# Kernel optimization log

Measured on AMD Instinct MI355X. Metric: run time of the kernel, lower is better.

Reference implementation:

```python
import jax, jax.numpy as jnp
import numpy as np

W_, H_, D_ = 45, 30, 13
TEXT = 226
NVID = W_ * H_ * D_            # 17550 video tokens
L = TEXT + NVID                # 17776 total tokens
BLK = 128
NKEEP = 32
NBLK = (L + BLK - 1) // BLK    # 139 blocks
LPAD = NBLK * BLK              # 17792
LEVELS = (1, 2, 4, 8)
MASK_RATIOS = ((1, 0.0, 0.05), (2, 0.05, 0.15), (4, 0.15, 0.25), (8, 0.25, 0.5), (0, 0.5, 1.0))
NEG = -1e30

def _sgn(x):
    return (x > 0) - (x < 0)

def _gen3d(x, y, z, ax, ay, az, bx, by, bz, cx, cy, cz):
    w = abs(ax + ay + az); h = abs(bx + by + bz); d = abs(cx + cy + cz)
    dax, day, daz = _sgn(ax), _sgn(ay), _sgn(az)
    dbx, dby, dbz = _sgn(bx), _sgn(by), _sgn(bz)
    dcx, dcy, dcz = _sgn(cx), _sgn(cy), _sgn(cz)
    if h == 1 and d == 1:
        for _ in range(w):
            yield (x, y, z); x += dax; y += day; z += daz
        return
    if w == 1 and d == 1:
        for _ in range(h):
            yield (x, y, z); x += dbx; y += dby; z += dbz
        return
    if w == 1 and h == 1:
        for _ in range(d):
            yield (x, y, z); x += dcx; y += dcy; z += dcz
        return
    ax2, ay2, az2 = ax // 2, ay // 2, az // 2
    bx2, by2, bz2 = bx // 2, by // 2, bz // 2
    cx2, cy2, cz2 = cx // 2, cy // 2, cz // 2
    w2 = abs(ax2 + ay2 + az2); h2 = abs(bx2 + by2 + bz2); d2 = abs(cx2 + cy2 + cz2)
    if (w2 % 2) and (w > 2): ax2 += dax; ay2 += day; az2 += daz
    if (h2 % 2) and (h > 2): bx2 += dbx; by2 += dby; bz2 += dbz
    if (d2 % 2) and (d > 2): cx2 += dcx; cy2 += dcy; cz2 += dcz
    if (2 * w > 3 * h) and (2 * w > 3 * d):
        yield from _gen3d(x, y, z, ax2, ay2, az2, bx, by, bz, cx, cy, cz)
        yield from _gen3d(x + ax2, y + ay2, z + az2, ax - ax2, ay - ay2, az - az2, bx, by, bz, cx, cy, cz)
    elif 3 * h > 4 * d:
        yield from _gen3d(x, y, z, bx2, by2, bz2, cx, cy, cz, ax2, ay2, az2)
        yield from _gen3d(x + bx2, y + by2, z + bz2, ax, ay, az, bx - bx2, by - by2, bz - bz2, cx, cy, cz)
        yield from _gen3d(x + (ax - dax) + (bx2 - dbx), y + (ay - day) + (by2 - dby), z + (az - daz) + (bz2 - dbz), -bx2, -by2, -bz2, cx, cy, cz, -(ax - ax2), -(ay - ay2), -(az - az2))
    elif 3 * d > 4 * h:
        yield from _gen3d(x, y, z, cx2, cy2, cz2, ax2, ay2, az2, bx, by, bz)
        yield from _gen3d(x + cx2, y + cy2, z + cz2, ax, ay, az, bx, by, bz, cx - cx2, cy - cy2, cz - cz2)
        yield from _gen3d(x + (ax - dax) + (cx2 - dcx), y + (ay - day) + (cy2 - dcy), z + (az - daz) + (cz2 - dcz), -cx2, -cy2, -cz2, -(ax - ax2), -(ay - ay2), -(az - az2), bx, by, bz)
    else:
        yield from _gen3d(x, y, z, bx2, by2, bz2, cx2, cy2, cz2, ax2, ay2, az2)
        yield from _gen3d(x + bx2, y + by2, z + bz2, cx, cy, cz, ax2, ay2, az2, bx - bx2, by - by2, bz - bz2)
        yield from _gen3d(x + (bx2 - dbx) + (cx - dcx), y + (by2 - dby) + (cy - dcy), z + (bz2 - dbz) + (cz - dcz), ax, ay, az, -bx2, -by2, -bz2, -(cx - cx2), -(cy - cy2), -(cz - cz2))
        yield from _gen3d(x + (ax - dax) + bx2 + (cx - dcx), y + (ay - day) + by2 + (cy - dcy), z + (az - daz) + bz2 + (cz - dcz), -cx, -cy, -cz, -(ax - ax2), -(ay - ay2), -(az - az2), bx - bx2, by - by2, bz - bz2)

def _gilbert3d(w, h, d):
    if w >= h and w >= d:
        yield from _gen3d(0, 0, 0, w, 0, 0, 0, h, 0, 0, 0, d)
    elif h >= w and h >= d:
        yield from _gen3d(0, 0, 0, 0, h, 0, w, 0, 0, 0, 0, d)
    else:
        yield from _gen3d(0, 0, 0, 0, 0, d, w, 0, 0, 0, h, 0)

def _perms():
    o2g = np.zeros(NVID, np.int64); g2o = np.zeros(NVID, np.int64)
    for g, (x, y, z) in enumerate(_gilbert3d(W_, H_, D_)):
        c = x + W_ * (y + H_ * z)
        o2g[g] = c; g2o[c] = g
    return jnp.asarray(o2g), jnp.asarray(g2o)

O2G, G2O = _perms()

def _sample(x, key):
    # random_sample_tokens: same NKEEP indices (per b,h) reused for every block
    B, Hh, _, Dd = x.shape
    r = jax.random.uniform(key, (B, Hh, BLK))
    idx = jax.lax.top_k(r, NKEEP)[1]                    # [B,H,NKEEP]
    xb = x.reshape(B, Hh, NBLK, BLK, Dd)
    s = jnp.take_along_axis(xb, idx[:, :, None, :, None], axis=3)
    return s.reshape(B, Hh, NBLK * NKEEP, Dd)

def _make_mask(q, k):
    # torch.no_grad() mask path
    q = jax.lax.stop_gradient(q); k = jax.lax.stop_gradient(k)
    pad = LPAD - L
    qp = jnp.pad(q, ((0, 0), (0, 0), (0, pad), (0, 0)), mode='edge')
    kp = jnp.pad(k, ((0, 0), (0, 0), (0, pad), (0, 0)), mode='edge')
    kq, kk = jax.random.split(jax.random.key(0))
    sq = _sample(qp, kq); sk = _sample(kp, kk)
    scale = 1.0 / float(np.sqrt(q.shape[-1]))
    attn = jax.nn.softmax(jnp.einsum('bhid,bhjd->bhij', sq, sk) * scale, axis=-1)
    B, Hh = attn.shape[:2]
    # sum-pool NKEEP x NKEEP -> block-level pooled attention [B,H,NBLK,NBLK]
    pool = attn.reshape(B, Hh, NBLK, NKEEP, NBLK, NKEEP).sum(axis=(3, 5))
    # rank of each column within its row (descending) == scatter over sorted indices
    rank = jnp.argsort(jnp.argsort(-pool, axis=-1), axis=-1)
    mask = jnp.zeros(pool.shape, jnp.int32)
    for val, s, e in MASK_RATIOS:
        si = max(0, int(NBLK * s)); ei = min(NBLK, int(NBLK * e))
        if si < ei and val != 0:
            mask = jnp.where((rank >= si) & (rank < ei), jnp.int32(val), mask)
    mask = mask.at[:, :, :, -2:].set(1)
    mask = mask.at[:, :, -2:, :].set(1)
    return mask

def _pooled_kv(kp, vp):
    # per-level mean-pooled K/V per key block, padded to BLK slots + log-count bias
    B, Hh, _, Dd = kp.shape
    valid = (jnp.arange(LPAD) < L).astype(kp.dtype).reshape(NBLK, BLK)
    kb = kp.reshape(B, Hh, NBLK, BLK, Dd)
    vb = vp.reshape(B, Hh, NBLK, BLK, Dd)
    Ks, Vs, Bs = [], [], []
    for m in LEVELS:
        g = BLK // m
        cnt = valid.reshape(NBLK, g, m).sum(-1)          # [NBLK,g] valid tokens per group
        den = jnp.maximum(cnt, 1.0)
        kpl = kb.reshape(B, Hh, NBLK, g, m, Dd).sum(4) / den[None, None, :, :, None]
        vpl = vb.reshape(B, Hh, NBLK, g, m, Dd).sum(4) / den[None, None, :, :, None]
        bias = jnp.where(cnt > 0, jnp.log(den), NEG)
        padn = BLK - g
        Ks.append(jnp.pad(kpl, ((0, 0), (0, 0), (0, 0), (0, padn), (0, 0))))
        Vs.append(jnp.pad(vpl, ((0, 0), (0, 0), (0, 0), (0, padn), (0, 0))))
        Bs.append(jnp.pad(bias, ((0, 0), (0, padn)), constant_values=NEG))
    return jnp.stack(Ks, 3), jnp.stack(Vs, 3), jnp.stack(Bs, 1)

def _sparse_attn(q, k, v, mask):
    B, Hh, _, Dd = q.shape
    pad = LPAD - L
    zp = ((0, 0), (0, 0), (0, pad), (0, 0))
    qp = jnp.pad(q, zp); kp = jnp.pad(k, zp); vp = jnp.pad(v, zp)
    KL, VL, BIAS = _pooled_kv(kp, vp)   # [B,H,NBLK,4,BLK,D], bias [NBLK,4,BLK]
    table = np.zeros(9, np.int32)
    table[1], table[2], table[4], table[8] = 0, 1, 2, 3
    lvl = jnp.asarray(table)[mask]
    act = mask > 0
    scale = 1.0 / float(np.sqrt(Dd))
    qb = jnp.transpose(qp.reshape(B, Hh, NBLK, BLK, Dd), (2, 0, 1, 3, 4))
    lvl_t = jnp.transpose(lvl, (2, 0, 1, 3))
    act_t = jnp.transpose(act, (2, 0, 1, 3))
    biasB = jnp.broadcast_to(BIAS[None, None], (B, Hh, NBLK, len(LEVELS), BLK))
    def body(carry, xs):
        qi, li, ai = xs                 # [B,H,BLK,D], [B,H,NBLK], [B,H,NBLK]
        sel = li[:, :, :, None, None]
        Ksel = jnp.take_along_axis(KL, sel[..., None], axis=3)[:, :, :, 0]   # [B,H,NBLK,BLK,D]
        Vsel = jnp.take_along_axis(VL, sel[..., None], axis=3)[:, :, :, 0]
        bsel = jnp.take_along_axis(biasB, sel, axis=3)[:, :, :, 0]           # [B,H,NBLK,BLK]
        logit = jnp.einsum('bhqd,bhknd->bhqkn', qi, Ksel) * scale
        logit = logit + jnp.where(ai[:, :, None, :, None], bsel[:, :, None], NEG)
        p = jax.nn.softmax(logit.reshape(B, Hh, BLK, NBLK * BLK), axis=-1)
        o = jnp.einsum('bhqn,bhnd->bhqd', p, Vsel.reshape(B, Hh, NBLK * BLK, Dd))
        return carry, o
    body = jax.checkpoint(body)
    _, outs = jax.lax.scan(body, None, (qb, lvl_t, act_t))
    out = jnp.transpose(outs, (1, 2, 0, 3, 4)).reshape(B, Hh, LPAD, Dd)
    return out[:, :, :L]

def _forward(q, k, v):
    def rearr(x):
        return jnp.concatenate([x[:, :, TEXT:][:, :, O2G], x[:, :, :TEXT]], axis=2)
    qr, kr, vr = rearr(q), rearr(k), rearr(v)
    mask = _make_mask(qr, kr)
    outr = _sparse_attn(qr, kr, vr, mask)
    return jnp.concatenate([outr[:, :, -TEXT:], outr[:, :, :-TEXT][:, :, G2O]], axis=2)

def setup_inputs():
    key = jax.random.key(0)
    kq, kk, kv = jax.random.split(key, 3)
    shp = (1, 8, L, 64)
    return {'q': jax.random.normal(kq, shp, jnp.float32),
            'k': jax.random.normal(kk, shp, jnp.float32),
            'v': jax.random.normal(kv, shp, jnp.float32)}

def reference(q, k, v):
    return _forward(q, k, v)
```

## Files before the change

kernel.cpp:

```cpp
#include <hip/hip_runtime.h>
#include <stdint.h>
#include <string.h>
#include <stdlib.h>

#define JAX_PARTITIONABLE 1

namespace {

constexpr int kW = 45, kH = 30, kD = 13;
constexpr int NVID = kW * kH * kD;
constexpr int TEXT = 226;
constexpr int LSEQ = TEXT + NVID;
constexpr int BLKSZ = 128;
constexpr int NBLK = 139;
constexpr int LPAD = NBLK * BLKSZ;
constexpr int NKEEP = 32;
constexpr int NS = NBLK * NKEEP;
constexpr int NH = 8;
constexpr int DD = 64;
constexpr int VLAST = LSEQ - (NBLK - 1) * BLKSZ;
constexpr float SCALE = 0.125f;
constexpr float SC2 = 0.18033688011120542f;
constexpr int MAXG = 188;

constexpr int NGR_H = LPAD / 16;
constexpr int NRAWG = NH * NGR_H;
constexpr int NPOOLG = NH * NBLK * 7;
constexpr int NGALL = NRAWG + NPOOLG;

constexpr int NSPLIT = 16;
constexpr int HCHUNK = (LSEQ + 63) / 64;
constexpr int CHPER = (HCHUNK + NSPLIT - 1) / NSPLIT;
constexpr int NHEAVYB = NH * 2 * NSPLIT;
constexpr int NLIGHT2 = NH * (NBLK - 2) * 2;

constexpr long SZ_RB = (long)NH * LPAD * DD / 2;
constexpr long SZ_SH = (long)NH * NS * DD / 2;
constexpr long SZ_KPB = (long)NH * NBLK * 112 * DD / 2;
constexpr long SZ_KF = (long)NGALL * 1024 / 2;
constexpr long SZ_VF = (long)NGALL * 1024 / 2;
constexpr long SZ_PL = (long)NH * NBLK * NBLK;
constexpr long SZ_O  = (long)NH * LSEQ * DD;
constexpr long SZ_PT = (long)NH * 2 * NSPLIT * BLKSZ * DD;
constexpr long SZ_PS = (long)NH * 2 * NSPLIT * BLKSZ;
constexpr long F_QB = 0;
constexpr long F_KB = F_QB + SZ_RB;
constexpr long F_VB = F_KB + SZ_RB;
constexpr long F_SQH = F_VB + SZ_RB;
constexpr long F_SQM = F_SQH + SZ_SH;
constexpr long F_SQL = F_SQM + SZ_SH;
constexpr long F_SKH = F_SQL + SZ_SH;
constexpr long F_SKM = F_SKH + SZ_SH;
constexpr long F_SKL = F_SKM + SZ_SH;
constexpr long F_KPB = F_SKL + SZ_SH;
constexpr long F_VPB = F_KPB + SZ_KPB;
constexpr long F_KFA = F_VPB + SZ_KPB;
constexpr long F_VFA = F_KFA + SZ_KF;
constexpr long F_PL = F_VFA + SZ_VF;
constexpr long F_MK = F_PL + SZ_PL;
constexpr long F_OR = F_MK + SZ_PL;
constexpr long F_PT = F_OR + SZ_O;
constexpr long F_PS = F_PT + SZ_PT;
constexpr long F_TB = F_PS + SZ_PS;
constexpr int TAB_INTS = 2 * LSEQ + 2 * NH * NKEEP;

struct Gil { int* out; int n; };
static inline int sgn_i(int v) { return (v > 0) - (v < 0); }
static inline int fd2(int a) { return a >= 0 ? a / 2 : -((-a + 1) / 2); }

static void gen3d(Gil& G, int x, int y, int z,
                  int ax, int ay, int az,
                  int bx, int by, int bz,
                  int cx, int cy, int cz) {
  int w = abs(ax + ay + az), h = abs(bx + by + bz), d = abs(cx + cy + cz);
  int dax = sgn_i(ax), day = sgn_i(ay), daz = sgn_i(az);
  int dbx = sgn_i(bx), dby = sgn_i(by), dbz = sgn_i(bz);
  int dcx = sgn_i(cx), dcy = sgn_i(cy), dcz = sgn_i(cz);
  if (h == 1 && d == 1) { for (int i = 0; i < w; i++) { G.out[G.n++] = x + kW * (y + kH * z); x += dax; y += day; z += daz; } return; }
  if (w == 1 && d == 1) { for (int i = 0; i < h; i++) { G.out[G.n++] = x + kW * (y + kH * z); x += dbx; y += dby; z += dbz; } return; }
  if (w == 1 && h == 1) { for (int i = 0; i < d; i++) { G.out[G.n++] = x + kW * (y + kH * z); x += dcx; y += dcy; z += dcz; } return; }
  int ax2 = fd2(ax), ay2 = fd2(ay), az2 = fd2(az);
  int bx2 = fd2(bx), by2 = fd2(by), bz2 = fd2(bz);
  int cx2 = fd2(cx), cy2 = fd2(cy), cz2 = fd2(cz);
  int w2 = abs(ax2 + ay2 + az2), h2 = abs(bx2 + by2 + bz2), d2 = abs(cx2 + cy2 + cz2);
  if ((w2 & 1) && w > 2) { ax2 += dax; ay2 += day; az2 += daz; }
  if ((h2 & 1) && h > 2) { bx2 += dbx; by2 += dby; bz2 += dbz; }
  if ((d2 & 1) && d > 2) { cx2 += dcx; cy2 += dcy; cz2 += dcz; }
  if (2 * w > 3 * h && 2 * w > 3 * d) {
    gen3d(G, x, y, z, ax2, ay2, az2, bx, by, bz, cx, cy, cz);
    gen3d(G, x + ax2, y + ay2, z + az2, ax - ax2, ay - ay2, az - az2, bx, by, bz, cx, cy, cz);
  } else if (3 * h > 4 * d) {
    gen3d(G, x, y, z, bx2, by2, bz2, cx, cy, cz, ax2, ay2, az2);
    gen3d(G, x + bx2, y + by2, z + bz2, ax, ay, az, bx - bx2, by - by2, bz - bz2, cx, cy, cz);
    gen3d(G, x + (ax - dax) + (bx2 - dbx), y + (ay - day) + (by2 - dby), z + (az - daz) + (bz2 - dbz),
          -bx2, -by2, -bz2, cx, cy, cz, -(ax - ax2), -(ay - ay2), -(az - az2));
  } else if (3 * d > 4 * h) {
    gen3d(G, x, y, z, cx2, cy2, cz2, ax2, ay2, az2, bx, by, bz);
    gen3d(G, x + cx2, y + cy2, z + cz2, ax, ay, az, bx, by, bz, cx - cx2, cy - cy2, cz - cz2);
    gen3d(G, x + (ax - dax) + (cx2 - dcx), y + (ay - day) + (cy2 - dcy), z + (az - daz) + (cz2 - dcz),
          -cx2, -cy2, -cz2, -(ax - ax2), -(ay - ay2), -(az - az2), bx, by, bz);
  } else {
    gen3d(G, x, y, z, bx2, by2, bz2, cx2, cy2, cz2, ax2, ay2, az2);
    gen3d(G, x + bx2, y + by2, z + bz2, cx, cy, cz, ax2, ay2, az2, bx - bx2, by - by2, bz - bz2);
    gen3d(G, x + (bx2 - dbx) + (cx - dcx), y + (by2 - dby) + (cy - dcy), z + (bz2 - dbz) + (cz - dcz),
          ax, ay, az, -bx2, -by2, -bz2, -(cx - cx2), -(cy - cy2), -(cz - cz2));
    gen3d(G, x + (ax - dax) + bx2 + (cx - dcx), y + (ay - day) + by2 + (cy - dcy), z + (az - daz) + bz2 + (cz - dcz),
          -cx, -cy, -cz, -(ax - ax2), -(ay - ay2), -(az - az2), bx - bx2, by - by2, bz - bz2);
  }
}

static void tf2x32(uint32_t k0, uint32_t k1, uint32_t x0, uint32_t x1,
                   uint32_t& o0, uint32_t& o1) {
  uint32_t ks0 = k0, ks1 = k1, ks2 = k0 ^ k1 ^ 0x1BD11BDAu;
  const uint32_t ks[3] = {ks0, ks1, ks2};
  const int rot[2][4] = {{13, 15, 26, 6}, {17, 29, 16, 24}};
  x0 += ks[0]; x1 += ks[1];
  for (int i = 0; i < 5; i++) {
    for (int j = 0; j < 4; j++) {
      int rr = rot[i & 1][j];
      x0 += x1;
      x1 = (x1 << rr) | (x1 >> (32 - rr));
      x1 ^= x0;
    }
    x0 += ks[(i + 1) % 3];
    x1 += ks[(i + 2) % 3] + (uint32_t)(i + 1);
  }
  o0 = x0; o1 = x1;
}

static inline float bits_to_unit(uint32_t bits) {
  uint32_t fb = (bits >> 9) | 0x3f800000u;
  float f; memcpy(&f, &fb, 4);
  return f - 1.0f;
}

static void fill_idx(uint32_t K0, uint32_t K1, int* dst) {
  float u[NH * BLKSZ];
#if JAX_PARTITIONABLE
  for (int i = 0; i < NH * BLKSZ; i++) {
    uint32_t a, b; tf2x32(K0, K1, 0u, (uint32_t)i, a, b);
    u[i] = bits_to_unit(a ^ b);
  }
#else
  {
    const int n = NH * BLKSZ, hn = n / 2;
    for (int i = 0; i < hn; i++) {
      uint32_t a, b; tf2x32(K0, K1, (uint32_t)i, (uint32_t)(hn + i), a, b);
      u[i] = bits_to_unit(a);
      u[hn + i] = bits_to_unit(b);
    }
  }
#endif
  for (int h = 0; h < NH; h++) {
    const float* row = u + h * BLKSZ;
    bool used[BLKSZ] = {false};
    for (int r = 0; r < NKEEP; r++) {
      int best = -1; float bv = -2.0f;
      for (int g = 0; g < BLKSZ; g++)
        if (!used[g] && row[g] > bv) { bv = row[g]; best = g; }
      used[best] = true;
      dst[h * NKEEP + r] = best;
    }
  }
}

static void build_tables(int* tab) {
  static int yields[NVID];
  static int o2g_buf[NVID];
  static int g2o_buf[NVID];
  memset(o2g_buf, 0, sizeof(o2g_buf));
  memset(g2o_buf, 0, sizeof(g2o_buf));
  Gil G{yields, 0};
  gen3d(G, 0, 0, 0, kW, 0, 0, 0, kH, 0, 0, 0, kD);
  int n = G.n;
  if (n > NVID) n = NVID;
  for (int g = 0; g < n; g++) o2g_buf[g] = yields[g];
  for (int g = 0; g < n; g++) g2o_buf[yields[g]] = g;

  int* inmap = tab;
  int* outg  = tab + LSEQ;
  for (int g = 0; g < NVID; g++) inmap[g] = TEXT + o2g_buf[g];
  for (int t = 0; t < TEXT; t++) inmap[NVID + t] = t;
  for (int r = 0; r < TEXT; r++) outg[r] = NVID + r;
  for (int c = 0; c < NVID; c++) outg[TEXT + c] = g2o_buf[c];

  uint32_t kq0, kq1, kk0, kk1;
#if JAX_PARTITIONABLE
  tf2x32(0, 0, 0, 0, kq0, kq1);
  tf2x32(0, 0, 0, 1, kk0, kk1);
#else
  {
    uint32_t y00, y10, y01, y11;
    tf2x32(0, 0, 0, 2, y00, y10);
    tf2x32(0, 0, 1, 3, y01, y11);
    kq0 = y00; kq1 = y01; kk0 = y10; kk1 = y11;
  }
#endif
  fill_idx(kq0, kq1, tab + 2 * LSEQ);
  fill_idx(kk0, kk1, tab + 2 * LSEQ + NH * NKEEP);
}

}


typedef __attribute__((ext_vector_type(8))) short short8v;
typedef __attribute__((ext_vector_type(4))) float f32x4;

static __device__ inline unsigned short f2bf(float f) {
  unsigned u = __float_as_uint(f);
  unsigned r = u + 0x7FFFu + ((u >> 16) & 1u);
  return (unsigned short)(r >> 16);
}
static __device__ inline float bf2f(unsigned short s) {
  return __uint_as_float(((unsigned)s) << 16);
}
static __device__ inline int cvtpk(float lo, float hi) {
  int r;
  asm("v_cvt_pk_bf16_f32 %0, %1, %2" : "=v"(r) : "v"(lo), "v"(hi));
  return r;
}

struct KFrag {
  short8v h[2][2], m[2][2], l[2][2];
};


__global__ __launch_bounds__(256) void k_rearr(
    const float* __restrict__ q, const float* __restrict__ k, const float* __restrict__ v,
    short* __restrict__ qrb, short* __restrict__ krb, short* __restrict__ vrb,
    const int* __restrict__ inmap) {
  long gid = (long)blockIdx.x * 256 + threadIdx.x;
  const long totalRows = 3L * NH * LPAD;
  long rowid = gid >> 3;
  int g8 = (int)(gid & 7);
  if (rowid >= totalRows) return;
  int tsel = (int)(rowid / ((long)NH * LPAD));
  long rem = rowid - (long)tsel * NH * LPAD;
  int h = (int)(rem / LPAD);
  int i = (int)(rem % LPAD);
  const float* src = tsel == 0 ? q : (tsel == 1 ? k : v);
  short8v outv;
  if (i < LSEQ) {
    const float* sp = src + ((long)h * LSEQ + inmap[i]) * DD + g8 * 8;
    float4 a = *(const float4*)sp;
    float4 b = *(const float4*)(sp + 4);
    float vals[8] = {a.x, a.y, a.z, a.w, b.x, b.y, b.z, b.w};
#pragma unroll
    for (int j = 0; j < 8; j++) outv[j] = (short)f2bf(vals[j]);
  } else {
#pragma unroll
    for (int j = 0; j < 8; j++) outv[j] = 0;
  }
  short* dst = tsel == 0 ? qrb : (tsel == 1 ? krb : vrb);
  *(short8v*)(dst + ((long)h * LPAD + i) * DD + g8 * 8) = outv;
}

__global__ __launch_bounds__(256) void k_sample(
    const float* __restrict__ q, const float* __restrict__ k,
    short* __restrict__ sqh, short* __restrict__ sqm, short* __restrict__ sql,
    short* __restrict__ skh, short* __restrict__ skm, short* __restrict__ skl,
    const int* __restrict__ qidx, const int* __restrict__ kidx,
    const int* __restrict__ inmap) {
  long gid = (long)blockIdx.x * 256 + threadIdx.x;
  int g = (int)(gid & 7);
  long rowid = gid >> 3;
  const long half = (long)NH * NS;
  if (rowid >= 2 * half) return;
  int tsel = rowid >= half;
  long rem = tsel ? rowid - half : rowid;
  int h = (int)(rem / NS);
  int s = (int)(rem % NS);
  int b = s / NKEEP, t = s % NKEEP;
  const int* idx = tsel ? kidx : qidx;
  int p = b * BLKSZ + idx[h * NKEEP + t];
  if (p >= LSEQ) p = LSEQ - 1;
  int orig = inmap[p];
  const float* src = (tsel ? k : q) + ((long)h * LSEQ + orig) * DD + g * 8;
  float4 a = *(const float4*)src;
  float4 bb = *(const float4*)(src + 4);
  float vals[8] = {a.x, a.y, a.z, a.w, bb.x, bb.y, bb.z, bb.w};
  short8v vh, vm, vl;
#pragma unroll
  for (int j = 0; j < 8; j++) {
    unsigned short hi = f2bf(vals[j]);
    float r1 = vals[j] - bf2f(hi);
    unsigned short mi = f2bf(r1);
    float r2 = r1 - bf2f(mi);
    unsigned short lo = f2bf(r2);
    vh[j] = (short)hi; vm[j] = (short)mi; vl[j] = (short)lo;
  }
  int t16 = s >> 4, lm = s & 15, ks = g >> 2, lg = g & 3;
  long off = (long)h * NS * DD + ((long)(t16 * 2 + ks)) * 512 + (lg * 16 + lm) * 8;
  if (tsel) {
    *(short8v*)(skh + off) = vh;
    *(short8v*)(skm + off) = vm;
    *(short8v*)(skl + off) = vl;
  } else {
    *(short8v*)(sqh + off) = vh;
    *(short8v*)(sqm + off) = vm;
    *(short8v*)(sql + off) = vl;
  }
}

static __device__ inline void ld_frags(
    const short* __restrict__ skh, const short* __restrict__ skm,
    const short* __restrict__ skl, long kbase, int c, int lane, KFrag& F) {
#pragma unroll
  for (int nt = 0; nt < 2; nt++)
#pragma unroll
    for (int ks = 0; ks < 2; ks++) {
      long a = kbase + ((long)((2 * c + nt) * 2 + ks)) * 512 + lane * 8;
      F.h[nt][ks] = *(const short8v*)(skh + a);
      F.m[nt][ks] = *(const short8v*)(skm + a);
      F.l[nt][ks] = *(const short8v*)(skl + a);
    }
}

__global__ __launch_bounds__(256, 2) void k_scores_pool(
    const short* __restrict__ sqh, const short* __restrict__ sqm, const short* __restrict__ sql,
    const short* __restrict__ skh, const short* __restrict__ skm, const short* __restrict__ skl,
    float* __restrict__ pool) {
  __shared__ float bins[32][145];
  __shared__ float invden[32];
  int bid = blockIdx.x;
  int h = bid & 7, qb = bid >> 3;
  int tid = threadIdx.x;
  int wid = tid >> 6, lane = tid & 63;
  int lm = lane & 15, lg = lane >> 4;

  for (int i = tid; i < 32 * 145; i += 256) (&bins[0][0])[i] = 0.f;

  const long base = (long)h * NS * DD;
  short8v Qh[2][2], Qm[2][2], Ql[2][2];
#pragma unroll
  for (int mt = 0; mt < 2; mt++)
#pragma unroll
    for (int ks = 0; ks < 2; ks++) {
      long off = base + ((long)((2 * qb + mt) * 2 + ks)) * 512 + lane * 8;
      Qh[mt][ks] = *(const short8v*)(sqh + off);
      Qm[mt][ks] = *(const short8v*)(sqm + off);
      Ql[mt][ks] = *(const short8v*)(sql + off);
    }
  __syncthreads();

  auto compute = [&](const KFrag& F, int c) {
    f32x4 aq[2][2];
#pragma unroll
    for (int mt = 0; mt < 2; mt++)
#pragma unroll
      for (int nt = 0; nt < 2; nt++) {
        f32x4 a = {0.f, 0.f, 0.f, 0.f};
#pragma unroll
        for (int ks = 0; ks < 2; ks++) {
          a = __builtin_amdgcn_mfma_f32_16x16x32_bf16(F.h[nt][ks], Qh[mt][ks], a, 0, 0, 0);
          a = __builtin_amdgcn_mfma_f32_16x16x32_bf16(F.h[nt][ks], Qm[mt][ks], a, 0, 0, 0);
          a = __builtin_amdgcn_mfma_f32_16x16x32_bf16(F.m[nt][ks], Qh[mt][ks], a, 0, 0, 0);
          a = __builtin_amdgcn_mfma_f32_16x16x32_bf16(F.m[nt][ks], Qm[mt][ks], a, 0, 0, 0);
          a = __builtin_amdgcn_mfma_f32_16x16x32_bf16(F.h[nt][ks], Ql[mt][ks], a, 0, 0, 0);
          a = __builtin_amdgcn_mfma_f32_16x16x32_bf16(F.l[nt][ks], Qh[mt][ks], a, 0, 0, 0);
        }
        aq[mt][nt] = a;
      }
#pragma unroll
    for (int mt = 0; mt < 2; mt++) {
      float s = 0.f;
#pragma unroll
      for (int nt = 0; nt < 2; nt++)
#pragma unroll
        for (int i = 0; i < 4; i++)
          s += __expf(aq[mt][nt][i] * SCALE);
      s += __shfl_xor(s, 16);
      s += __shfl_xor(s, 32);
      if (lg == 0) bins[mt * 16 + lm][c] += s;
    }
  };

  KFrag A, B;
  ld_frags(skh, skm, skl, base, wid, lane, A);
  for (int c = wid; c < NBLK; c += 8) {
    if (c + 4 < NBLK) ld_frags(skh, skm, skl, base, c + 4, lane, B);
    compute(A, c);
    if (c + 4 >= NBLK) break;
    if (c + 8 < NBLK) ld_frags(skh, skm, skl, base, c + 8, lane, A);
    compute(B, c + 4);
  }

  __syncthreads();
  if (tid < 32) {
    float s = 0.f;
    for (int kb = 0; kb < NBLK; kb++) s += bins[tid][kb];
    invden[tid] = 1.0f / s;
  }
  __syncthreads();
  if (tid < NBLK) {
    float s = 0.f;
    for (int r2 = 0; r2 < NKEEP; r2++) s += bins[r2][tid] * invden[r2];
    pool[((long)h * NBLK + qb) * NBLK + tid] = s;
  }
}

__global__ __launch_bounds__(192) void k_mask(
    const float* __restrict__ pool, int* __restrict__ mask) {
  __shared__ float row[NBLK];
  int h = blockIdx.x / NBLK, i = blockIdx.x % NBLK;
  int t = threadIdx.x;
  const float* pr = pool + ((long)h * NBLK + i) * NBLK;
  if (t < NBLK) row[t] = pr[t];
  __syncthreads();
  if (t < NBLK) {
    float pv = row[t];
    int rank = 0;
    for (int j = 0; j < NBLK; j++) {
      float o = row[j];
      rank += (o > pv) || (o == pv && j < t);
    }
    int val = 0;
    if (rank < 6) val = 1;
    else if (rank < 20) val = 2;
    else if (rank < 34) val = 4;
    else if (rank < 69) val = 8;
    if (t >= NBLK - 2) val = 1;
    if (i >= NBLK - 2) val = 1;
    mask[((long)h * NBLK + i) * NBLK + t] = val;
  }
}

__global__ __launch_bounds__(256) void k_poolkv(
    const short* __restrict__ krb, const short* __restrict__ vrb,
    short* __restrict__ Kpb, short* __restrict__ Vpb) {
  long rid = (long)blockIdx.x * 4 + (threadIdx.x >> 6);
  int d = threadIdx.x & 63;
  const long total = 2L * NH * NBLK * 112;
  if (rid >= total) return;
  int tsel = (int)(rid / ((long)NH * NBLK * 112));
  long rem = rid - (long)tsel * NH * NBLK * 112;
  int h = (int)(rem / (NBLK * 112));
  int rem2 = (int)(rem % (NBLK * 112));
  int j = rem2 / 112, p = rem2 % 112;
  int m, g;
  if (p < 64) { m = 2; g = p; }
  else if (p < 96) { m = 4; g = p - 64; }
  else { m = 8; g = p - 96; }
  const short* src = tsel ? vrb : krb;
  const short* base = src + ((long)h * LPAD + j * BLKSZ + g * m) * DD + d;
  float sum = 0.f;
  for (int r2 = 0; r2 < m; r2++) sum += bf2f((unsigned short)base[(long)r2 * DD]);
  short* dst = tsel ? Vpb : Kpb;
  dst[(((long)h * NBLK + j) * 112 + p) * DD + d] = (short)f2bf(sum / (float)m);
}

__global__ __launch_bounds__(256) void k_fragk(
    const short* __restrict__ krb, const short* __restrict__ Kpb,
    short* __restrict__ kfAll) {
  long gid = (long)blockIdx.x * 256 + threadIdx.x;
  if (gid >= (long)NGALL * 128) return;
  int lane = (int)(gid & 63);
  int ks = (int)((gid >> 6) & 1);
  long grp = gid >> 7;
  int lm = lane & 15, lg = lane >> 4;
  const short* srcp;
  long row;
  if (grp < NRAWG) { srcp = krb; row = grp * 16 + lm; }
  else { srcp = Kpb; row = (grp - NRAWG) * 16 + lm; }
  short8v vv = *(const short8v*)(srcp + row * DD + ks * 32 + lg * 8);
  *(short8v*)(kfAll + ((long)grp * 2 + ks) * 512 + lane * 8) = vv;
}

__global__ __launch_bounds__(256) void k_fragv(
    const short* __restrict__ vrb, const short* __restrict__ Vpb,
    short* __restrict__ vfAll) {
  long gid = (long)blockIdx.x * 256 + threadIdx.x;
  if (gid >= (long)NGALL * 256) return;
  int lane = (int)(gid & 63);
  int mtp = (int)((gid >> 6) & 3);
  long grp = gid >> 8;
  int lm = lane & 15, lg = lane >> 4;
  const short* srcp;
  long rowb;
  if (grp < NRAWG) { srcp = vrb; rowb = grp * 16 + lg * 4; }
  else { srcp = Vpb; rowb = (grp - NRAWG) * 16 + lg * 4; }
  short4 o;
  o.x = srcp[(rowb + 0) * DD + mtp * 16 + lm];
  o.y = srcp[(rowb + 1) * DD + mtp * 16 + lm];
  o.z = srcp[(rowb + 2) * DD + mtp * 16 + lm];
  o.w = srcp[(rowb + 3) * DD + mtp * 16 + lm];
  *(short4*)(vfAll + ((long)grp * 4 + mtp) * 256 + lane * 4) = o;
}

__global__ __launch_bounds__(256, 2) void k_attn_light(
    const short* __restrict__ qrb,
    const short* __restrict__ kfAll, const short* __restrict__ vfAll,
    const int* __restrict__ mask,
    float* __restrict__ outr) {
  __shared__ int glist[MAXG];
  __shared__ int wtot[4];
  __shared__ int smeta;
  __shared__ __align__(16) short KtF[4096];
  __shared__ __align__(16) short VtF[4096];

  int bid = blockIdx.x;
  int half = bid & 1;
  int lb = bid >> 1;
  int h = lb / (NBLK - 2);
  int qi = lb % (NBLK - 2);
  int tid = threadIdx.x;
  int lane = tid & 63, wid = tid >> 6;
  int lm = lane & 15, lg = lane >> 4;

  int myng = 0, mylvl = 0, myG = 0;
  if (tid < NBLK) {
    int mv = mask[((long)h * NBLK + qi) * NBLK + tid];
    if (mv) {
      mylvl = (mv == 1) ? 0 : (mv == 2) ? 1 : (mv == 4) ? 2 : 3;
      myG = ((tid == NBLK - 1) ? VLAST : BLKSZ) >> mylvl;
      myng = (myG + 15) >> 4;
    }
  }
  int v = myng;
#pragma unroll
  for (int off = 1; off < 64; off <<= 1) {
    int t2 = __shfl_up(v, off);
    if ((tid & 63) >= off) v += t2;
  }
  if ((tid & 63) == 63) wtot[wid] = v;
  __syncthreads();
  int woff = 0;
#pragma unroll
  for (int w = 0; w < 4; w++) if (w < wid) woff += wtot[w];
  int myoff = woff + v - myng;
  if (tid == 0) {
    int tot = wtot[0] + wtot[1] + wtot[2] + wtot[3];
    while (tot & 3) glist[tot++] = 0;
    smeta = tot >> 2;
  }
  __syncthreads();
  if (tid < NBLK && myng) {
    int grp0;
    if (mylvl == 0) grp0 = h * NGR_H + tid * 8;
    else {
      int l16 = (mylvl == 1) ? 0 : (mylvl == 2) ? 4 : 6;
      grp0 = NRAWG + (h * NBLK + tid) * 7 + l16;
    }
    for (int g = 0; g < myng; g++) {
      int cnt = myG - 16 * g; if (cnt > 16) cnt = 16;
      glist[myoff + g] = (grp0 + g) | (cnt << 24) | (mylvl << 29);
    }
  }
  __syncthreads();
  int nchunks = smeta;

  short8v Qf[2];
  {
    long row = (long)h * LPAD + qi * BLKSZ + half * 64 + wid * 16 + lm;
    Qf[0] = *(const short8v*)(qrb + row * DD + lg * 8);
    Qf[1] = *(const short8v*)(qrb + row * DD + 32 + lg * 8);
  }
  short8v onesv;
#pragma unroll
  for (int j = 0; j < 8; j++) onesv[j] = (short)0x3F80;
  f32x4 Oacc[4];
#pragma unroll
  for (int a = 0; a < 4; a++) { f32x4 z = {0.f, 0.f, 0.f, 0.f}; Oacc[a] = z; }
  f32x4 Oden = {0.f, 0.f, 0.f, 0.f};

  short8v rk0, rk1, rv0, rv1;
  auto ldStage = [&](int c) {
    {
      int s = tid;
      long grp = (long)((unsigned)glist[4 * c + (s >> 7)] & 0xFFFFFFu);
      rk0 = *(const short8v*)(kfAll + (grp * 2 + ((s >> 6) & 1)) * 512 + (long)(s & 63) * 8);
      s = tid + 256;
      grp = (long)((unsigned)glist[4 * c + (s >> 7)] & 0xFFFFFFu);
      rk1 = *(const short8v*)(kfAll + (grp * 2 + ((s >> 6) & 1)) * 512 + (long)(s & 63) * 8);
    }
    {
      int s = tid;
      long grp = (long)((unsigned)glist[4 * c + (s >> 7)] & 0xFFFFFFu);
      rv0 = *(const short8v*)(vfAll + (grp * 4 + ((s >> 5) & 3)) * 256 + (long)(s & 31) * 8);
      s = tid + 256;
      grp = (long)((unsigned)glist[4 * c + (s >> 7)] & 0xFFFFFFu);
      rv1 = *(const short8v*)(vfAll + (grp * 4 + ((s >> 5) & 3)) * 256 + (long)(s & 31) * 8);
    }
  };
  auto stStage = [&]() {
    *(short8v*)&KtF[tid * 8] = rk0;
    *(short8v*)&KtF[(tid + 256) * 8] = rk1;
    {
      int s = tid;
      int g = s >> 7, mtp = (s >> 5) & 3, l = s & 31;
      int base = (mtp * 2 + (g >> 1)) * 512 + ((g & 1) * 4) + l * 16;
      *(short4*)&VtF[base] = make_short4(rv0[0], rv0[1], rv0[2], rv0[3]);
      *(short4*)&VtF[base + 8] = make_short4(rv0[4], rv0[5], rv0[6], rv0[7]);
      s = tid + 256;
      g = s >> 7; mtp = (s >> 5) & 3; l = s & 31;
      base = (mtp * 2 + (g >> 1)) * 512 + ((g & 1) * 4) + l * 16;
      *(short4*)&VtF[base] = make_short4(rv1[0], rv1[1], rv1[2], rv1[3]);
      *(short4*)&VtF[base + 8] = make_short4(rv1[4], rv1[5], rv1[6], rv1[7]);
    }
  };

  ldStage(0);
  for (int c = 0; c < nchunks; c++) {
    __syncthreads();
    stStage();
    __syncthreads();
    if (c + 1 < nchunks) ldStage(c + 1);

    int cntv[4]; float biasv[4];
#pragma unroll
    for (int g = 0; g < 4; g++) {
      unsigned e = (unsigned)glist[4 * c + g];
      cntv[g] = (e >> 24) & 31;
      biasv[g] = (float)((e >> 29) & 3);
    }
    bool allfull = (cntv[0] == 16) & (cntv[1] == 16) & (cntv[2] == 16) & (cntv[3] == 16);

    f32x4 aq[4];
#pragma unroll
    for (int nt = 0; nt < 4; nt++) {
      short8v k0 = *(short8v*)&KtF[(nt * 2 + 0) * 512 + lane * 8];
      short8v k1 = *(short8v*)&KtF[(nt * 2 + 1) * 512 + lane * 8];
      f32x4 z = {0.f, 0.f, 0.f, 0.f};
      f32x4 a = __builtin_amdgcn_mfma_f32_16x16x32_bf16(k0, Qf[0], z, 0, 0, 0);
      aq[nt] = __builtin_amdgcn_mfma_f32_16x16x32_bf16(k1, Qf[1], a, 0, 0, 0);
    }
    float ps[16];
    if (allfull) {
#pragma unroll
      for (int nt = 0; nt < 4; nt++)
#pragma unroll
        for (int i = 0; i < 4; i++)
          ps[nt * 4 + i] = exp2f(fmaf(aq[nt][i], SC2, biasv[nt]));
    } else {
#pragma unroll
      for (int nt = 0; nt < 4; nt++)
#pragma unroll
        for (int i = 0; i < 4; i++) {
          int kvr = lg * 4 + i;
          ps[nt * 4 + i] = (kvr < cntv[nt]) ? exp2f(fmaf(aq[nt][i], SC2, biasv[nt])) : 0.f;
        }
    }
    short8v Pf[2];
#pragma unroll
    for (int H = 0; H < 2; H++) {
      union { int i[4]; short8v v; } u;
      u.i[0] = cvtpk(ps[8 * H + 0], ps[8 * H + 1]);
      u.i[1] = cvtpk(ps[8 * H + 2], ps[8 * H + 3]);
      u.i[2] = cvtpk(ps[8 * H + 4], ps[8 * H + 5]);
      u.i[3] = cvtpk(ps[8 * H + 6], ps[8 * H + 7]);
      Pf[H] = u.v;
    }
    Oden = __builtin_amdgcn_mfma_f32_16x16x32_bf16(onesv, Pf[0], Oden, 0, 0, 0);
    Oden = __builtin_amdgcn_mfma_f32_16x16x32_bf16(onesv, Pf[1], Oden, 0, 0, 0);
#pragma unroll
    for (int mtp = 0; mtp < 4; mtp++) {
      short8v vf0 = *(short8v*)&VtF[(mtp * 2 + 0) * 512 + lane * 8];
      short8v vf1 = *(short8v*)&VtF[(mtp * 2 + 1) * 512 + lane * 8];
      Oacc[mtp] = __builtin_amdgcn_mfma_f32_16x16x32_bf16(vf0, Pf[0], Oacc[mtp], 0, 0, 0);
      Oacc[mtp] = __builtin_amdgcn_mfma_f32_16x16x32_bf16(vf1, Pf[1], Oacc[mtp], 0, 0, 0);
    }
  }

  float inv = 1.0f / Oden[0];
  {
    int grow = qi * BLKSZ + half * 64 + wid * 16 + lm;
    float* orow = outr + ((long)h * LSEQ + grow) * DD;
#pragma unroll
    for (int mtp = 0; mtp < 4; mtp++) {
      f32x4 o = Oacc[mtp];
      *(float4*)(orow + mtp * 16 + lg * 4) =
          make_float4(o[0] * inv, o[1] * inv, o[2] * inv, o[3] * inv);
    }
  }
}

__global__ __launch_bounds__(256, 1) void k_attn_heavy(
    const short* __restrict__ qrb, const short* __restrict__ krb,
    const short* __restrict__ vrb,
    float* __restrict__ part, float* __restrict__ plsum) {
  __shared__ __align__(16) short Kt[64 * 64];
  __shared__ __align__(16) short Vt[64 * 68];

  int bid = blockIdx.x;
  int split = bid & (NSPLIT - 1);
  int hq = bid / NSPLIT;
  int h = hq >> 1;
  int qi = NBLK - 2 + (hq & 1);
  int c0 = split * CHPER;
  int c1 = c0 + CHPER; if (c1 > HCHUNK) c1 = HCHUNK;
  int slot = hq * NSPLIT + split;
  int tid = threadIdx.x;

  int lane = tid & 63, wid = tid >> 6;
  int lm = lane & 15, lg = lane >> 4;

  short8v Qf[2][2];
#pragma unroll
  for (int mt = 0; mt < 2; mt++)
#pragma unroll
    for (int ks = 0; ks < 2; ks++) {
      long row = (long)h * LPAD + qi * BLKSZ + wid * 32 + mt * 16 + lm;
      Qf[mt][ks] = *(const short8v*)(qrb + row * DD + ks * 32 + lg * 8);
    }

  f32x4 Oacc[4][2];
#pragma unroll
  for (int a = 0; a < 4; a++)
#pragma unroll
    for (int b = 0; b < 2; b++) { f32x4 z = {0.f, 0.f, 0.f, 0.f}; Oacc[a][b] = z; }
  float lrow0 = 0.f, lrow1 = 0.f;

  int sr = tid & 63;
  int sd0 = (tid >> 6) * 16;

  short8v pkA, pkB, pvA, pvB;
  {
    long src = (long)h * LPAD + (long)c0 * 64 + sr;
    const short8v* kp = (const short8v*)(krb + src * DD + sd0);
    const short8v* vp = (const short8v*)(vrb + src * DD + sd0);
    pkA = kp[0]; pkB = kp[1];
    pvA = vp[0]; pvB = vp[1];
  }

  for (int c = c0; c < c1; c++) {
    __syncthreads();
    {
      int sw = (sr & 7) << 3;
      *(short8v*)&Kt[sr * 64 + (sd0 ^ sw)] = pkA;
      *(short8v*)&Kt[sr * 64 + ((sd0 + 8) ^ sw)] = pkB;
#pragma unroll
      for (int i = 0; i < 8; i++) {
        Vt[(sd0 + i) * 68 + sr] = pvA[i];
        Vt[(sd0 + 8 + i) * 68 + sr] = pvB[i];
      }
    }
    __syncthreads();
    if (c + 1 < c1) {
      long src = (long)h * LPAD + (long)(c + 1) * 64 + sr;
      const short8v* kp = (const short8v*)(krb + src * DD + sd0);
      const short8v* vp = (const short8v*)(vrb + src * DD + sd0);
      pkA = kp[0]; pkB = kp[1];
      pvA = vp[0]; pvB = vp[1];
    }

    bool allfull = (c != HCHUNK - 1);

    short8v Kf[4][2];
#pragma unroll
    for (int nt = 0; nt < 4; nt++)
#pragma unroll
      for (int ks = 0; ks < 2; ks++)
        Kf[nt][ks] = *(short8v*)&Kt[(nt * 16 + lm) * 64 + ((ks * 32 + lg * 8) ^ ((lm & 7) << 3))];

    short8v Pf[2][2];
#pragma unroll
    for (int mt = 0; mt < 2; mt++) {
      f32x4 aq[4];
#pragma unroll
      for (int nt = 0; nt < 4; nt++) {
        f32x4 z = {0.f, 0.f, 0.f, 0.f};
        f32x4 a = __builtin_amdgcn_mfma_f32_16x16x32_bf16(Kf[nt][0], Qf[mt][0], z, 0, 0, 0);
        aq[nt] = __builtin_amdgcn_mfma_f32_16x16x32_bf16(Kf[nt][1], Qf[mt][1], a, 0, 0, 0);
      }
      float ps[16];
      if (allfull) {
#pragma unroll
        for (int nt = 0; nt < 4; nt++)
#pragma unroll
          for (int i = 0; i < 4; i++)
            ps[nt * 4 + i] = __expf(aq[nt][i] * SCALE);
      } else {
#pragma unroll
        for (int nt = 0; nt < 4; nt++) {
          int cc = LSEQ - 16 * (4 * c + nt);
          int cnt = cc <= 0 ? 0 : (cc >= 16 ? 16 : cc);
#pragma unroll
          for (int i = 0; i < 4; i++) {
            int kvr = lg * 4 + i;
            ps[nt * 4 + i] = (kvr < cnt) ? __expf(aq[nt][i] * SCALE) : 0.f;
          }
        }
      }
      float lsum = 0.f;
#pragma unroll
      for (int i = 0; i < 16; i++) lsum += ps[i];
      if (mt == 0) lrow0 += lsum; else lrow1 += lsum;
#pragma unroll
      for (int H = 0; H < 2; H++) {
        union { int i[4]; short8v v; } u;
        u.i[0] = cvtpk(ps[8 * H + 0], ps[8 * H + 1]);
        u.i[1] = cvtpk(ps[8 * H + 2], ps[8 * H + 3]);
        u.i[2] = cvtpk(ps[8 * H + 4], ps[8 * H + 5]);
        u.i[3] = cvtpk(ps[8 * H + 6], ps[8 * H + 7]);
        Pf[mt][H] = u.v;
      }
    }

#pragma unroll
    for (int mtp = 0; mtp < 4; mtp++) {
      int d68 = (mtp * 16 + lm) * 68;
#pragma unroll
      for (int H = 0; H < 2; H++) {
        short4 lo = *(short4*)&Vt[d68 + H * 32 + lg * 4];
        short4 hi = *(short4*)&Vt[d68 + H * 32 + 16 + lg * 4];
        short8v vf;
        vf[0] = lo.x; vf[1] = lo.y; vf[2] = lo.z; vf[3] = lo.w;
        vf[4] = hi.x; vf[5] = hi.y; vf[6] = hi.z; vf[7] = hi.w;
        Oacc[mtp][0] = __builtin_amdgcn_mfma_f32_16x16x32_bf16(vf, Pf[0][H], Oacc[mtp][0], 0, 0, 0);
        Oacc[mtp][1] = __builtin_amdgcn_mfma_f32_16x16x32_bf16(vf, Pf[1][H], Oacc[mtp][1], 0, 0, 0);
      }
    }
  }

  lrow0 += __shfl_xor(lrow0, 16); lrow0 += __shfl_xor(lrow0, 32);
  lrow1 += __shfl_xor(lrow1, 16); lrow1 += __shfl_xor(lrow1, 32);
  if (lg == 0) {
    plsum[(long)slot * BLKSZ + wid * 32 + lm] = lrow0;
    plsum[(long)slot * BLKSZ + wid * 32 + 16 + lm] = lrow1;
  }
#pragma unroll
  for (int mt = 0; mt < 2; mt++) {
    int lrow = wid * 32 + mt * 16 + lm;
    float* orow = part + ((long)slot * BLKSZ + lrow) * DD;
#pragma unroll
    for (int mtp = 0; mtp < 4; mtp++) {
      f32x4 o = Oacc[mtp][mt];
      *(float4*)(orow + mtp * 16 + lg * 4) = make_float4(o[0], o[1], o[2], o[3]);
    }
  }
}

__global__ __launch_bounds__(256) void k_combine(
    const float* __restrict__ part, const float* __restrict__ plsum,
    float* __restrict__ outr) {
  int hq = blockIdx.x;
  int h = hq >> 1;
  int qi = NBLK - 2 + (hq & 1);
  int t = threadIdx.x;
  int row = t >> 1;
  int dbase = (t & 1) * 32;
  float l = 0.f;
  for (int s = 0; s < NSPLIT; s++) l += plsum[(long)(hq * NSPLIT + s) * BLKSZ + row];
  int grow = qi * BLKSZ + row;
  if (grow >= LSEQ) return;
  float inv = 1.0f / l;
  float* orow = outr + ((long)h * LSEQ + grow) * DD;
  for (int d = dbase; d < dbase + 32; d += 4) {
    float4 acc = make_float4(0.f, 0.f, 0.f, 0.f);
    for (int s = 0; s < NSPLIT; s++) {
      float4 p4 = *(const float4*)&part[((long)(hq * NSPLIT + s) * BLKSZ + row) * DD + d];
      acc.x += p4.x; acc.y += p4.y; acc.z += p4.z; acc.w += p4.w;
    }
    *(float4*)(orow + d) = make_float4(acc.x * inv, acc.y * inv, acc.z * inv, acc.w * inv);
  }
}

__global__ __launch_bounds__(256) void k_out(
    const float* __restrict__ outr, const int* __restrict__ outg,
    float* __restrict__ out) {
  long rid = (long)blockIdx.x * 4 + (threadIdx.x >> 6);
  int d = threadIdx.x & 63;
  const long total = (long)NH * LSEQ;
  if (rid >= total) return;
  int h = (int)(rid / LSEQ);
  int r = (int)(rid % LSEQ);
  int src = outg[r];
  out[((long)h * LSEQ + r) * DD + d] = outr[((long)h * LSEQ + src) * DD + d];
}


extern "C" void kernel_launch(void* const* d_in, const int* in_sizes, int n_in,
                              void* d_out, int out_size, void* d_ws, size_t ws_size,
                              hipStream_t stream) {
  (void)in_sizes; (void)n_in; (void)out_size; (void)ws_size;
  const float* q = (const float*)d_in[0];
  const float* k = (const float*)d_in[1];
  const float* v = (const float*)d_in[2];
  float* ws = (float*)d_ws;
  float* out = (float*)d_out;

  static int* htab = nullptr;
  if (!htab) { (void)hipHostMalloc((void**)&htab, TAB_INTS * sizeof(int)); }
  build_tables(htab);

  int* dtab = (int*)(ws + F_TB);
  int* inmap = dtab;
  int* outg = dtab + LSEQ;
  int* qidx = dtab + 2 * LSEQ;
  int* kidx = qidx + NH * NKEEP;
  int* dmask = (int*)(ws + F_MK);
  short* qrb = (short*)(ws + F_QB);
  short* krb = (short*)(ws + F_KB);
  short* vrb = (short*)(ws + F_VB);
  short* sqh = (short*)(ws + F_SQH);
  short* sqm = (short*)(ws + F_SQM);
  short* sql = (short*)(ws + F_SQL);
  short* skh = (short*)(ws + F_SKH);
  short* skm = (short*)(ws + F_SKM);
  short* skl = (short*)(ws + F_SKL);
  short* Kpb = (short*)(ws + F_KPB);
  short* Vpb = (short*)(ws + F_VPB);
  short* kfAll = (short*)(ws + F_KFA);
  short* vfAll = (short*)(ws + F_VFA);
  float* pool = ws + F_PL;
  float* outr = ws + F_OR;
  float* part = ws + F_PT;
  float* plsum = ws + F_PS;

  hipMemcpyAsync(dtab, htab, TAB_INTS * sizeof(int), hipMemcpyHostToDevice, stream);

  {
    long thr = 3L * NH * LPAD * 8;
    k_rearr<<<dim3((unsigned)((thr + 255) / 256)), 256, 0, stream>>>(
        q, k, v, qrb, krb, vrb, inmap);
  }
  {
    long thr = 2L * NH * NS * 8;
    k_sample<<<dim3((unsigned)((thr + 255) / 256)), 256, 0, stream>>>(
        q, k, sqh, sqm, sql, skh, skm, skl, qidx, kidx, inmap);
  }
  k_scores_pool<<<dim3(NH * NBLK), 256, 0, stream>>>(
      sqh, sqm, sql, skh, skm, skl, pool);
  k_mask<<<dim3(NH * NBLK), 192, 0, stream>>>(pool, dmask);
  {
    long rows = 2L * NH * NBLK * 112;
    k_poolkv<<<dim3((unsigned)((rows + 3) / 4)), 256, 0, stream>>>(krb, vrb, Kpb, Vpb);
  }
  {
    long thr = (long)NGALL * 128;
    k_fragk<<<dim3((unsigned)((thr + 255) / 256)), 256, 0, stream>>>(krb, Kpb, kfAll);
  }
  {
    long thr = (long)NGALL * 256;
    k_fragv<<<dim3((unsigned)((thr + 255) / 256)), 256, 0, stream>>>(vrb, Vpb, vfAll);
  }
  k_attn_heavy<<<dim3(NHEAVYB), 256, 0, stream>>>(qrb, krb, vrb, part, plsum);
  k_attn_light<<<dim3(NLIGHT2), 256, 0, stream>>>(qrb, kfAll, vfAll, dmask, outr);
  k_combine<<<dim3(NH * 2), 256, 0, stream>>>(part, plsum, outr);
  {
    long rows = (long)NH * LSEQ;
    k_out<<<dim3((unsigned)((rows + 3) / 4)), 256, 0, stream>>>(outr, outg, out);
  }
}
```

Baseline: 488.3 us.

## Scatter attention output directly to final rows and double-buffer light-kernel LDS

New measurement: 493.3 us. Within noise of the previous version (+1.0%).

```diff
diff --git a/kernel.cpp b/kernel.cpp
--- a/kernel.cpp
+++ b/kernel.cpp
@@ -40,7 +40,6 @@
 constexpr long SZ_KF = (long)NGALL * 1024 / 2;
 constexpr long SZ_VF = (long)NGALL * 1024 / 2;
 constexpr long SZ_PL = (long)NH * NBLK * NBLK;
-constexpr long SZ_O  = (long)NH * LSEQ * DD;
 constexpr long SZ_PT = (long)NH * 2 * NSPLIT * BLKSZ * DD;
 constexpr long SZ_PS = (long)NH * 2 * NSPLIT * BLKSZ;
 constexpr long F_QB = 0;
@@ -58,11 +57,10 @@
 constexpr long F_VFA = F_KFA + SZ_KF;
 constexpr long F_PL = F_VFA + SZ_VF;
 constexpr long F_MK = F_PL + SZ_PL;
-constexpr long F_OR = F_MK + SZ_PL;
-constexpr long F_PT = F_OR + SZ_O;
+constexpr long F_PT = F_MK + SZ_PL;
 constexpr long F_PS = F_PT + SZ_PT;
 constexpr long F_TB = F_PS + SZ_PS;
-constexpr int TAB_INTS = 2 * LSEQ + 2 * NH * NKEEP;
+constexpr int TAB_MAX = 2 * LSEQ + 2 * NH * NKEEP + 2 * NVID;
 
 struct Gil { int* out; int n; };
 static inline int sgn_i(int v) { return (v > 0) - (v < 0); }
@@ -164,10 +162,13 @@
   }
 }
 
+static int g_ndup = 0;
+
 static void build_tables(int* tab) {
   static int yields[NVID];
   static int o2g_buf[NVID];
   static int g2o_buf[NVID];
+  static int outg_loc[LSEQ];
   memset(o2g_buf, 0, sizeof(o2g_buf));
   memset(g2o_buf, 0, sizeof(g2o_buf));
   Gil G{yields, 0};
@@ -178,11 +179,24 @@
   for (int g = 0; g < n; g++) g2o_buf[yields[g]] = g;
 
   int* inmap = tab;
-  int* outg  = tab + LSEQ;
+  int* dstrow = tab + LSEQ;
+  int* qidx = tab + 2 * LSEQ;
+  int* kidx = qidx + NH * NKEEP;
+  int* duppairs = kidx + NH * NKEEP;
+
   for (int g = 0; g < NVID; g++) inmap[g] = TEXT + o2g_buf[g];
   for (int t = 0; t < TEXT; t++) inmap[NVID + t] = t;
-  for (int r = 0; r < TEXT; r++) outg[r] = NVID + r;
-  for (int c = 0; c < NVID; c++) outg[TEXT + c] = g2o_buf[c];
+  for (int r = 0; r < TEXT; r++) outg_loc[r] = NVID + r;
+  for (int c = 0; c < NVID; c++) outg_loc[TEXT + c] = g2o_buf[c];
+
+  for (int g = 0; g < LSEQ; g++) dstrow[g] = -1;
+  int nd = 0;
+  for (int r = 0; r < LSEQ; r++) {
+    int g = outg_loc[r];
+    if (dstrow[g] < 0) dstrow[g] = r;
+    else { duppairs[2 * nd] = r; duppairs[2 * nd + 1] = dstrow[g]; nd++; }
+  }
+  g_ndup = nd;
 
   uint32_t kq0, kq1, kk0, kk1;
 #if JAX_PARTITIONABLE
@@ -196,8 +210,8 @@
     kq0 = y00; kq1 = y01; kk0 = y10; kk1 = y11;
   }
 #endif
-  fill_idx(kq0, kq1, tab + 2 * LSEQ);
-  fill_idx(kk0, kk1, tab + 2 * LSEQ + NH * NKEEP);
+  fill_idx(kq0, kq1, qidx);
+  fill_idx(kk0, kk1, kidx);
 }
 
 }
@@ -490,13 +504,13 @@
 __global__ __launch_bounds__(256, 2) void k_attn_light(
     const short* __restrict__ qrb,
     const short* __restrict__ kfAll, const short* __restrict__ vfAll,
-    const int* __restrict__ mask,
-    float* __restrict__ outr) {
+    const int* __restrict__ mask, const int* __restrict__ dstrow,
+    float* __restrict__ out) {
   __shared__ int glist[MAXG];
   __shared__ int wtot[4];
   __shared__ int smeta;
-  __shared__ __align__(16) short KtF[4096];
-  __shared__ __align__(16) short VtF[4096];
+  __shared__ __align__(16) short KtF[2][4096];
+  __shared__ __align__(16) short VtF[2][4096];
 
   int bid = blockIdx.x;
   int half = bid & 1;
@@ -582,29 +596,33 @@
       rv1 = *(const short8v*)(vfAll + (grp * 4 + ((s >> 5) & 3)) * 256 + (long)(s & 31) * 8);
     }
   };
-  auto stStage = [&]() {
-    *(short8v*)&KtF[tid * 8] = rk0;
-    *(short8v*)&KtF[(tid + 256) * 8] = rk1;
+  auto stStage = [&](int wb) {
+    *(short8v*)&KtF[wb][tid * 8] = rk0;
+    *(short8v*)&KtF[wb][(tid + 256) * 8] = rk1;
     {
       int s = tid;
       int g = s >> 7, mtp = (s >> 5) & 3, l = s & 31;
       int base = (mtp * 2 + (g >> 1)) * 512 + ((g & 1) * 4) + l * 16;
-      *(short4*)&VtF[base] = make_short4(rv0[0], rv0[1], rv0[2], rv0[3]);
-      *(short4*)&VtF[base + 8] = make_short4(rv0[4], rv0[5], rv0[6], rv0[7]);
+      *(short4*)&VtF[wb][base] = make_short4(rv0[0], rv0[1], rv0[2], rv0[3]);
+      *(short4*)&VtF[wb][base + 8] = make_short4(rv0[4], rv0[5], rv0[6], rv0[7]);
       s = tid + 256;
       g = s >> 7; mtp = (s >> 5) & 3; l = s & 31;
       base = (mtp * 2 + (g >> 1)) * 512 + ((g & 1) * 4) + l * 16;
-      *(short4*)&VtF[base] = make_short4(rv1[0], rv1[1], rv1[2], rv1[3]);
-      *(short4*)&VtF[base + 8] = make_short4(rv1[4], rv1[5], rv1[6], rv1[7]);
+      *(short4*)&VtF[wb][base] = make_short4(rv1[0], rv1[1], rv1[2], rv1[3]);
+      *(short4*)&VtF[wb][base + 8] = make_short4(rv1[4], rv1[5], rv1[6], rv1[7]);
     }
   };
 
   ldStage(0);
+  stStage(0);
+  __syncthreads();
+  int buf = 0;
+
   for (int c = 0; c < nchunks; c++) {
-    __syncthreads();
-    stStage();
-    __syncthreads();
-    if (c + 1 < nchunks) ldStage(c + 1);
+    if (c + 1 < nchunks) {
+      ldStage(c + 1);
+      stStage(buf ^ 1);
+    }
 
     int cntv[4]; float biasv[4];
 #pragma unroll
@@ -618,8 +636,8 @@
     f32x4 aq[4];
 #pragma unroll
     for (int nt = 0; nt < 4; nt++) {
-      short8v k0 = *(short8v*)&KtF[(nt * 2 + 0) * 512 + lane * 8];
-      short8v k1 = *(short8v*)&KtF[(nt * 2 + 1) * 512 + lane * 8];
+      short8v k0 = *(short8v*)&KtF[buf][(nt * 2 + 0) * 512 + lane * 8];
+      short8v k1 = *(short8v*)&KtF[buf][(nt * 2 + 1) * 512 + lane * 8];
       f32x4 z = {0.f, 0.f, 0.f, 0.f};
       f32x4 a = __builtin_amdgcn_mfma_f32_16x16x32_bf16(k0, Qf[0], z, 0, 0, 0);
       aq[nt] = __builtin_amdgcn_mfma_f32_16x16x32_bf16(k1, Qf[1], a, 0, 0, 0);
@@ -654,22 +672,27 @@
     Oden = __builtin_amdgcn_mfma_f32_16x16x32_bf16(onesv, Pf[1], Oden, 0, 0, 0);
 #pragma unroll
     for (int mtp = 0; mtp < 4; mtp++) {
-      short8v vf0 = *(short8v*)&VtF[(mtp * 2 + 0) * 512 + lane * 8];
-      short8v vf1 = *(short8v*)&VtF[(mtp * 2 + 1) * 512 + lane * 8];
+      short8v vf0 = *(short8v*)&VtF[buf][(mtp * 2 + 0) * 512 + lane * 8];
+      short8v vf1 = *(short8v*)&VtF[buf][(mtp * 2 + 1) * 512 + lane * 8];
       Oacc[mtp] = __builtin_amdgcn_mfma_f32_16x16x32_bf16(vf0, Pf[0], Oacc[mtp], 0, 0, 0);
       Oacc[mtp] = __builtin_amdgcn_mfma_f32_16x16x32_bf16(vf1, Pf[1], Oacc[mtp], 0, 0, 0);
     }
+    __syncthreads();
+    buf ^= 1;
   }
 
   float inv = 1.0f / Oden[0];
   {
     int grow = qi * BLKSZ + half * 64 + wid * 16 + lm;
-    float* orow = outr + ((long)h * LSEQ + grow) * DD;
-#pragma unroll
-    for (int mtp = 0; mtp < 4; mtp++) {
-      f32x4 o = Oacc[mtp];
-      *(float4*)(orow + mtp * 16 + lg * 4) =
-          make_float4(o[0] * inv, o[1] * inv, o[2] * inv, o[3] * inv);
+    int dr = dstrow[grow];
+    if (dr >= 0) {
+      float* orow = out + ((long)h * LSEQ + dr) * DD;
+#pragma unroll
+      for (int mtp = 0; mtp < 4; mtp++) {
+        f32x4 o = Oacc[mtp];
+        *(float4*)(orow + mtp * 16 + lg * 4) =
+            make_float4(o[0] * inv, o[1] * inv, o[2] * inv, o[3] * inv);
+      }
     }
   }
 }
@@ -832,7 +855,7 @@
 
 __global__ __launch_bounds__(256) void k_combine(
     const float* __restrict__ part, const float* __restrict__ plsum,
-    float* __restrict__ outr) {
+    const int* __restrict__ dstrow, float* __restrict__ out) {
   int hq = blockIdx.x;
   int h = hq >> 1;
   int qi = NBLK - 2 + (hq & 1);
@@ -843,8 +866,10 @@
   for (int s = 0; s < NSPLIT; s++) l += plsum[(long)(hq * NSPLIT + s) * BLKSZ + row];
   int grow = qi * BLKSZ + row;
   if (grow >= LSEQ) return;
+  int dr = dstrow[grow];
+  if (dr < 0) return;
   float inv = 1.0f / l;
-  float* orow = outr + ((long)h * LSEQ + grow) * DD;
+  float* orow = out + ((long)h * LSEQ + dr) * DD;
   for (int d = dbase; d < dbase + 32; d += 4) {
     float4 acc = make_float4(0.f, 0.f, 0.f, 0.f);
     for (int s = 0; s < NSPLIT; s++) {
@@ -855,17 +880,16 @@
   }
 }
 
-__global__ __launch_bounds__(256) void k_out(
-    const float* __restrict__ outr, const int* __restrict__ outg,
-    float* __restrict__ out) {
-  long rid = (long)blockIdx.x * 4 + (threadIdx.x >> 6);
-  int d = threadIdx.x & 63;
-  const long total = (long)NH * LSEQ;
-  if (rid >= total) return;
-  int h = (int)(rid / LSEQ);
-  int r = (int)(rid % LSEQ);
-  int src = outg[r];
-  out[((long)h * LSEQ + r) * DD + d] = outr[((long)h * LSEQ + src) * DD + d];
+__global__ __launch_bounds__(64) void k_fixup(
+    const int* __restrict__ duppairs, float* __restrict__ out, int nd) {
+  int bid = blockIdx.x;
+  int h = bid & (NH - 1);
+  int dup = bid >> 3;
+  if (dup >= nd) return;
+  int rdst = duppairs[2 * dup];
+  int rsrc = duppairs[2 * dup + 1];
+  out[((long)h * LSEQ + rdst) * DD + threadIdx.x] =
+      out[((long)h * LSEQ + rsrc) * DD + threadIdx.x];
 }
 
 
@@ -880,14 +904,16 @@
   float* out = (float*)d_out;
 
   static int* htab = nullptr;
-  if (!htab) { (void)hipHostMalloc((void**)&htab, TAB_INTS * sizeof(int)); }
+  if (!htab) { (void)hipHostMalloc((void**)&htab, TAB_MAX * sizeof(int)); }
   build_tables(htab);
+  int ndup = g_ndup;
 
   int* dtab = (int*)(ws + F_TB);
   int* inmap = dtab;
-  int* outg = dtab + LSEQ;
+  int* dstrow = dtab + LSEQ;
   int* qidx = dtab + 2 * LSEQ;
   int* kidx = qidx + NH * NKEEP;
+  int* duppairs = kidx + NH * NKEEP;
   int* dmask = (int*)(ws + F_MK);
   short* qrb = (short*)(ws + F_QB);
   short* krb = (short*)(ws + F_KB);
@@ -903,11 +929,12 @@
   short* kfAll = (short*)(ws + F_KFA);
   short* vfAll = (short*)(ws + F_VFA);
   float* pool = ws + F_PL;
-  float* outr = ws + F_OR;
   float* part = ws + F_PT;
   float* plsum = ws + F_PS;
 
-  hipMemcpyAsync(dtab, htab, TAB_INTS * sizeof(int), hipMemcpyHostToDevice, stream);
+  hipMemcpyAsync(dtab, htab,
+                 (size_t)(2 * LSEQ + 2 * NH * NKEEP + 2 * ndup) * sizeof(int),
+                 hipMemcpyHostToDevice, stream);
 
   {
     long thr = 3L * NH * LPAD * 8;
@@ -935,10 +962,9 @@
     k_fragv<<<dim3((unsigned)((thr + 255) / 256)), 256, 0, stream>>>(vrb, Vpb, vfAll);
   }
   k_attn_heavy<<<dim3(NHEAVYB), 256, 0, stream>>>(qrb, krb, vrb, part, plsum);
-  k_attn_light<<<dim3(NLIGHT2), 256, 0, stream>>>(qrb, kfAll, vfAll, dmask, outr);
-  k_combine<<<dim3(NH * 2), 256, 0, stream>>>(part, plsum, outr);
-  {
-    long rows = (long)NH * LSEQ;
-    k_out<<<dim3((unsigned)((rows + 3) / 4)), 256, 0, stream>>>(outr, outg, out);
-  }
-}
+  k_attn_light<<<dim3(NLIGHT2), 256, 0, stream>>>(qrb, kfAll, vfAll, dmask, dstrow, out);
+  k_combine<<<dim3(NH * 2), 256, 0, stream>>>(part, plsum, dstrow, out);
+  if (ndup > 0) {
+    k_fixup<<<dim3((unsigned)(ndup * NH)), 64, 0, stream>>>(duppairs, out, ndup);
+  }
+}
```
